# Kernel tuning notes

Measured on AMD Instinct MI355X. Metric: run time of the kernel, lower is better.

The kernel has to match this reference:

```python
import jax, jax.numpy as jnp
import numpy as np

B, C, T = 64, 1, 262144
NUM_BANDS = 6
# (min, max) for each of the 18 normalized control params: 6 bands x (gain_dB, cutoff_Hz, Q)
PARAM_RANGES = np.array([
    [-24.0, 24.0], [20.0, 200.0], [0.1, 10.0],      # low shelf
    [-24.0, 24.0], [200.0, 2000.0], [0.1, 10.0],    # band 1
    [-24.0, 24.0], [200.0, 2000.0], [0.1, 10.0],    # band 2
    [-24.0, 24.0], [2000.0, 8000.0], [0.1, 10.0],   # band 3
    [-24.0, 24.0], [4000.0, 12000.0], [0.1, 10.0],  # band 4
    [-24.0, 24.0], [4000.0, 12000.0], [0.1, 10.0],  # high shelf
], dtype=np.float32)
FILTER_TYPES = ["low_shelf", "peaking", "peaking", "peaking", "peaking", "high_shelf"]


def biquad_coeffs(gain_dB, cutoff, q, sr, ftype):
    # Audio-EQ-cookbook biquad coefficients; all inputs shape (B,)
    A = 10.0 ** (gain_dB / 40.0)
    w0 = 2.0 * jnp.pi * (cutoff / sr)
    alpha = jnp.sin(w0) / (2.0 * q)
    c = jnp.cos(w0)
    sA = jnp.sqrt(A)
    if ftype == "low_shelf":
        b0 = A * ((A + 1) - (A - 1) * c + 2 * sA * alpha)
        b1 = 2 * A * ((A - 1) - (A + 1) * c)
        b2 = A * ((A + 1) - (A - 1) * c - 2 * sA * alpha)
        a0 = (A + 1) + (A - 1) * c + 2 * sA * alpha
        a1 = -2 * ((A - 1) + (A + 1) * c)
        a2 = (A + 1) + (A - 1) * c - 2 * sA * alpha
    elif ftype == "high_shelf":
        b0 = A * ((A + 1) + (A - 1) * c + 2 * sA * alpha)
        b1 = -2 * A * ((A - 1) + (A + 1) * c)
        b2 = A * ((A + 1) + (A - 1) * c - 2 * sA * alpha)
        a0 = (A + 1) - (A - 1) * c + 2 * sA * alpha
        a1 = 2 * ((A - 1) - (A + 1) * c)
        a2 = (A + 1) - (A - 1) * c - 2 * sA * alpha
    else:  # peaking
        b0 = 1 + alpha * A
        b1 = -2 * c
        b2 = 1 - alpha * A
        a0 = 1 + alpha / A
        a1 = -2 * c
        a2 = 1 - alpha / A
    bcoef = jnp.stack([b0, b1, b2], axis=-1) / a0[..., None]  # (B, 3)
    acoef = jnp.stack([a0, a1, a2], axis=-1) / a0[..., None]  # (B, 3)
    return bcoef, acoef


def cascade_biquads(x, bcoefs, acoefs):
    # x: (N, T); bcoefs/acoefs: (6, N, 3). Fused cascade of 6 biquads,
    # direct form II transposed, single scan over time.
    def step(state, xt):  # state: (6, N, 2); xt: (N,)
        v = xt
        new_states = []
        for k in range(NUM_BANDS):
            bk, ak = bcoefs[k], acoefs[k]
            s1, s2 = state[k, :, 0], state[k, :, 1]
            y = bk[:, 0] * v + s1
            ns1 = bk[:, 1] * v - ak[:, 1] * y + s2
            ns2 = bk[:, 2] * v - ak[:, 2] * y
            new_states.append(jnp.stack([ns1, ns2], axis=-1))
            v = y
        return jnp.stack(new_states, axis=0), v
    init = jnp.zeros((NUM_BANDS, x.shape[0], 2), dtype=x.dtype)
    _, y = jax.lax.scan(step, init, x.T)  # y: (T, N)
    return y.T


def setup_inputs() -> dict:
    key = jax.random.key(0)
    k1, k2, k3 = jax.random.split(key, 3)
    x = jax.random.normal(k1, (B, C, T), dtype=jnp.float32) * 0.1
    p = jax.random.normal(k2, (B, 22), dtype=jnp.float32)
    W = jax.random.normal(k3, (18, 22), dtype=jnp.float32) * (1.0 / np.sqrt(22.0))
    b = jnp.zeros((18,), dtype=jnp.float32)
    return {"x": x, "p": p, "W": W, "b": b, "sample_rate": 24000}


def reference(x, p, W, b, sample_rate):
    bs, chs, s = x.shape
    sr = jnp.float32(sample_rate)
    # control path: linear + sigmoid -> 18 normalized params in [0, 1]
    pn = jax.nn.sigmoid(p @ W.T + b)  # (bs, 18)
    lo = jnp.asarray(PARAM_RANGES[:, 0])
    hi = jnp.asarray(PARAM_RANGES[:, 1])
    params = pn * (hi - lo) + lo  # denormalized, (bs, 18)
    bcoefs, acoefs = [], []
    for k, ftype in enumerate(FILTER_TYPES):
        g, f, q = params[:, 3 * k], params[:, 3 * k + 1], params[:, 3 * k + 2]
        bk, ak = biquad_coeffs(g, f, q, sr, ftype)
        bcoefs.append(bk)
        acoefs.append(ak)
    bcoefs = jnp.stack(bcoefs, axis=0)  # (6, bs, 3)
    acoefs = jnp.stack(acoefs, axis=0)
    # share each item's EQ across its channels
    bcoefs = jnp.repeat(bcoefs, chs, axis=1)  # (6, bs*chs, 3)
    acoefs = jnp.repeat(acoefs, chs, axis=1)
    y = cascade_biquads(x.reshape(bs * chs, s), bcoefs, acoefs)
    return y.reshape(bs, chs, s)
```

## Files before the change

kernel.cpp:

```cpp
#include <hip/hip_runtime.h>
#include <math.h>

#define NB    64
#define NT    262144
#define CH    64
#define NCK   (NT/CH)
#define NBANDS 6

#define COEF_OFF 0
#define MAT_OFF  4096
#define T_OFF    (MAT_OFF + NB*1728)
#define WPRE_OFF (T_OFF + NB*64*12)
#define D_OFF    (WPRE_OFF + NB*64*12)

struct Coef { float b0, b1, b2, a1, a2; };

__device__ __forceinline__ float rfl(float x) {
  return __int_as_float(__builtin_amdgcn_readfirstlane(__float_as_int(x)));
}

__device__ __forceinline__ float cascade_step(float v, float s[12], const Coef cf[NBANDS]) {
#pragma unroll
  for (int k = 0; k < NBANDS; ++k) {
    float s1 = s[2*k], s2 = s[2*k+1];
    float y   = fmaf(cf[k].b0, v, s1);
    float ns1 = fmaf(cf[k].b1, v, fmaf(-cf[k].a1, y, s2));
    float ns2 = fmaf(cf[k].b2, v, -cf[k].a2 * y);
    s[2*k]   = ns1;
    s[2*k+1] = ns2;
    v = y;
  }
  return v;
}

__device__ __forceinline__ void load_coefs(const float* ws, int batch, Coef cf[NBANDS]) {
  const float* c = ws + COEF_OFF + batch*30;
#pragma unroll
  for (int k = 0; k < NBANDS; ++k) {
    cf[k].b0 = rfl(c[5*k+0]); cf[k].b1 = rfl(c[5*k+1]); cf[k].b2 = rfl(c[5*k+2]);
    cf[k].a1 = rfl(c[5*k+3]); cf[k].a2 = rfl(c[5*k+4]);
  }
}

__global__ __launch_bounds__(64) void k_prep(const float* __restrict__ p, const float* __restrict__ W,
                                             const float* __restrict__ bias, const int* __restrict__ srp,
                                             float* __restrict__ ws) {
  __shared__ float prmS[18];
  __shared__ float cfS[30];
  __shared__ float M0[144], M1[144];
  int b = blockIdx.x, tid = threadIdx.x;
  const float lo[18] = {-24.f,20.f,0.1f,  -24.f,200.f,0.1f,  -24.f,200.f,0.1f,
                        -24.f,2000.f,0.1f, -24.f,4000.f,0.1f, -24.f,4000.f,0.1f};
  const float hi[18] = { 24.f,200.f,10.f,  24.f,2000.f,10.f,  24.f,2000.f,10.f,
                         24.f,8000.f,10.f, 24.f,12000.f,10.f, 24.f,12000.f,10.f};
  if (tid < 18) {
    float acc = bias[tid];
    for (int j = 0; j < 22; ++j) acc = fmaf(W[tid*22+j], p[b*22+j], acc);
    float sg = 1.f / (1.f + expf(-acc));
    prmS[tid] = sg * (hi[tid] - lo[tid]) + lo[tid];
  }
  __syncthreads();
  if (tid < 6) {
    int k = tid;
    float g = prmS[3*k], f = prmS[3*k+1], q = prmS[3*k+2];
    float sr = (float)srp[0];
    float A  = powf(10.f, g * (1.f/40.f));
    float w0 = 6.28318530717958647692f * (f / sr);
    float al = sinf(w0) / (2.f*q);
    float c  = cosf(w0);
    float sA = sqrtf(A);
    float b0,b1,b2,a0,a1,a2;
    if (k == 0) {
      b0 = A*((A+1.f) - (A-1.f)*c + 2.f*sA*al);
      b1 = 2.f*A*((A-1.f) - (A+1.f)*c);
      b2 = A*((A+1.f) - (A-1.f)*c - 2.f*sA*al);
      a0 = (A+1.f) + (A-1.f)*c + 2.f*sA*al;
      a1 = -2.f*((A-1.f) + (A+1.f)*c);
      a2 = (A+1.f) + (A-1.f)*c - 2.f*sA*al;
    } else if (k == 5) {
      b0 = A*((A+1.f) + (A-1.f)*c + 2.f*sA*al);
      b1 = -2.f*A*((A-1.f) + (A+1.f)*c);
      b2 = A*((A+1.f) + (A-1.f)*c - 2.f*sA*al);
      a0 = (A+1.f) - (A-1.f)*c + 2.f*sA*al;
      a1 = 2.f*((A-1.f) - (A+1.f)*c);
      a2 = (A+1.f) - (A-1.f)*c - 2.f*sA*al;
    } else {
      b0 = 1.f + al*A;
      b1 = -2.f*c;
      b2 = 1.f - al*A;
      a0 = 1.f + al/A;
      a1 = -2.f*c;
      a2 = 1.f - al/A;
    }
    float inv = 1.f/a0;
    float* cws = ws + COEF_OFF + b*30;
    cws[5*k+0] = cfS[5*k+0] = b0*inv;
    cws[5*k+1] = cfS[5*k+1] = b1*inv;
    cws[5*k+2] = cfS[5*k+2] = b2*inv;
    cws[5*k+3] = cfS[5*k+3] = a1*inv;
    cws[5*k+4] = cfS[5*k+4] = a2*inv;
  }
  __syncthreads();

  Coef cf[NBANDS];
#pragma unroll
  for (int k = 0; k < NBANDS; ++k) {
    cf[k].b0 = cfS[5*k+0]; cf[k].b1 = cfS[5*k+1]; cf[k].b2 = cfS[5*k+2];
    cf[k].a1 = cfS[5*k+3]; cf[k].a2 = cfS[5*k+4];
  }
  if (tid < 12) {
    float s[12];
#pragma unroll
    for (int r = 0; r < 12; ++r) s[r] = (r == tid) ? 1.f : 0.f;
    cascade_step(0.f, s, cf);
#pragma unroll
    for (int r = 0; r < 12; ++r) M0[r*12 + tid] = s[r];
  }
  __syncthreads();

  float* S = M0; float* D = M1;
  float* mout = ws + MAT_OFF + (size_t)b*1728;
  for (int q = 0; q < 6; ++q) {
    for (int e = tid; e < 144; e += 64) {
      int r = e/12, c = e%12;
      float acc = 0.f;
#pragma unroll
      for (int k = 0; k < 12; ++k) acc = fmaf(S[r*12+k], S[k*12+c], acc);
      D[e] = acc;
    }
    __syncthreads();
    float* t = S; S = D; D = t;
  }
  for (int e = tid; e < 144; e += 64) mout[e] = S[e];
  for (int l = 1; l < 12; ++l) {
    for (int e = tid; e < 144; e += 64) {
      int r = e/12, c = e%12;
      float acc = 0.f;
#pragma unroll
      for (int k = 0; k < 12; ++k) acc = fmaf(S[r*12+k], S[k*12+c], acc);
      D[e] = acc;
    }
    __syncthreads();
    float* t = S; S = D; D = t;
    for (int e = tid; e < 144; e += 64) mout[l*144 + e] = S[e];
  }
}

__global__ __launch_bounds__(256) void k_passA(const float* __restrict__ x, float* __restrict__ ws) {
  __shared__ float4 buf[4][2][256];
  __shared__ float KM[6][144];
  int tid = threadIdx.x, wib = tid >> 6, lane = tid & 63;
  int gw = blockIdx.x*4 + wib;
  int batch = gw >> 6, wv = gw & 63;
  int batch_b = blockIdx.x >> 4;

  const float* mb = ws + MAT_OFF + (size_t)batch_b*1728;
  for (int e = tid; e < 864; e += 256) KM[e/144][e%144] = mb[e];
  __syncthreads();

  const float4* x4 = (const float4*)x;
  size_t gbase4 = (size_t)batch*65536 + (size_t)wv*1024;
  int r2 = lane >> 2, c2 = lane & 3;
  float4* bufA = buf[wib][0];
  float4* bufB = buf[wib][1];

  float4 va[4], vb[4];
#pragma unroll
  for (int j = 0; j < 4; ++j) va[j] = x4[gbase4 + (size_t)(j*16 + r2)*16 + c2];

  Coef cf[NBANDS];
  load_coefs(ws, batch, cf);
  float s[12];
#pragma unroll
  for (int i = 0; i < 12; ++i) s[i] = 0.f;

#pragma unroll
  for (int j = 0; j < 4; ++j) bufA[c2*64 + j*16 + r2] = va[j];
  asm volatile("s_waitcnt lgkmcnt(0)" ::: "memory");

#pragma unroll
  for (int q = 0; q < 4; ++q) {
    float4* bp = (q & 1) ? bufB : bufA;
    float4* bn = (q & 1) ? bufA : bufB;
    float4* vr = (q & 1) ? va : vb;
    if (q < 3) {
#pragma unroll
      for (int j = 0; j < 4; ++j)
        vr[j] = x4[gbase4 + (size_t)(j*16 + r2)*16 + (q+1)*4 + c2];
    }
#pragma unroll
    for (int t = 0; t < 4; ++t) {
      float4 xv = bp[t*64 + lane];
      cascade_step(xv.x, s, cf);
      cascade_step(xv.y, s, cf);
      cascade_step(xv.z, s, cf);
      cascade_step(xv.w, s, cf);
    }
    if (q < 3) {
#pragma unroll
      for (int j = 0; j < 4; ++j) bn[c2*64 + j*16 + r2] = vr[j];
      asm volatile("s_waitcnt lgkmcnt(0)" ::: "memory");
    }
  }

#pragma unroll
  for (int l = 0; l < 6; ++l) {
    const int pd = 1 << l;
    float nb[12];
#pragma unroll
    for (int r = 0; r < 12; ++r) nb[r] = __shfl_up(s[r], pd);
    if (lane >= pd) {
#pragma unroll
      for (int r = 0; r < 12; ++r) {
        float acc = s[r];
#pragma unroll
        for (int c = 0; c < 12; ++c) acc = fmaf(KM[l][r*12+c], nb[c], acc);
        s[r] = acc;
      }
    }
  }

  if (lane == 63) {
    float4* tp = (float4*)(ws + T_OFF + ((size_t)batch*64 + wv)*12);
    tp[0] = make_float4(s[0], s[1], s[2],  s[3]);
    tp[1] = make_float4(s[4], s[5], s[6],  s[7]);
    tp[2] = make_float4(s[8], s[9], s[10], s[11]);
  }

  float e[12];
#pragma unroll
  for (int r = 0; r < 12; ++r) e[r] = __shfl_up(s[r], 1);
  if (lane == 0) {
#pragma unroll
    for (int r = 0; r < 12; ++r) e[r] = 0.f;
  }
  int chunk = wv*64 + lane;
  float4* dp = (float4*)(ws + D_OFF + ((size_t)batch*NCK + chunk)*12);
  dp[0] = make_float4(e[0], e[1], e[2],  e[3]);
  dp[1] = make_float4(e[4], e[5], e[6],  e[7]);
  dp[2] = make_float4(e[8], e[9], e[10], e[11]);
}

__global__ __launch_bounds__(64) void k_scanW(float* __restrict__ ws) {
  __shared__ float WM[6][144];
  int b = blockIdx.x, lane = threadIdx.x;
  const float* mb = ws + MAT_OFF + (size_t)b*1728 + 864;
  for (int e = lane; e < 864; e += 64) WM[e/144][e%144] = mb[e];
  __syncthreads();

  const float4* tp = (const float4*)(ws + T_OFF + ((size_t)b*64 + lane)*12);
  float4 a0 = tp[0], a1 = tp[1], a2 = tp[2];
  float s[12] = {a0.x,a0.y,a0.z,a0.w, a1.x,a1.y,a1.z,a1.w, a2.x,a2.y,a2.z,a2.w};

#pragma unroll
  for (int l = 0; l < 6; ++l) {
    const int pd = 1 << l;
    float nb[12];
#pragma unroll
    for (int r = 0; r < 12; ++r) nb[r] = __shfl_up(s[r], pd);
    if (lane >= pd) {
#pragma unroll
      for (int r = 0; r < 12; ++r) {
        float acc = s[r];
#pragma unroll
        for (int c = 0; c < 12; ++c) acc = fmaf(WM[l][r*12+c], nb[c], acc);
        s[r] = acc;
      }
    }
  }
  float e[12];
#pragma unroll
  for (int r = 0; r < 12; ++r) e[r] = __shfl_up(s[r], 1);
  if (lane == 0) {
#pragma unroll
    for (int r = 0; r < 12; ++r) e[r] = 0.f;
  }
  float4* wp = (float4*)(ws + WPRE_OFF + ((size_t)b*64 + lane)*12);
  wp[0] = make_float4(e[0], e[1], e[2],  e[3]);
  wp[1] = make_float4(e[4], e[5], e[6],  e[7]);
  wp[2] = make_float4(e[8], e[9], e[10], e[11]);
}

__global__ __launch_bounds__(256) void k_passB(const float* __restrict__ x, const float* __restrict__ ws,
                                               float* __restrict__ out) {
  __shared__ float4 buf[4][2][256];
  __shared__ float KM[6][144];
  int tid = threadIdx.x, wib = tid >> 6, lane = tid & 63;
  int gw = blockIdx.x*4 + wib;
  int batch = gw >> 6, wv = gw & 63;
  int batch_b = blockIdx.x >> 4;

  const float* mb = ws + MAT_OFF + (size_t)batch_b*1728;
  for (int e = tid; e < 864; e += 256) KM[e/144][e%144] = mb[e];
  __syncthreads();

  const float4* x4 = (const float4*)x;
  float4* out4 = (float4*)out;
  size_t gbase4 = (size_t)batch*65536 + (size_t)wv*1024;
  int r2 = lane >> 2, c2 = lane & 3;
  float4* bufA = buf[wib][0];
  float4* bufB = buf[wib][1];

  float4 va[4], vb[4];
#pragma unroll
  for (int j = 0; j < 4; ++j) va[j] = x4[gbase4 + (size_t)(j*16 + r2)*16 + c2];

  Coef cf[NBANDS];
  load_coefs(ws, batch, cf);

  int chunk = wv*64 + lane;
  const float4* dp = (const float4*)(ws + D_OFF + ((size_t)batch*NCK + chunk)*12);
  float4 e0 = dp[0], e1 = dp[1], e2 = dp[2];
  const float4* wp = (const float4*)(ws + WPRE_OFF + ((size_t)batch*64 + wv)*12);
  float4 w0 = wp[0], w1 = wp[1], w2 = wp[2];
  float R[12] = {w0.x,w0.y,w0.z,w0.w, w1.x,w1.y,w1.z,w1.w, w2.x,w2.y,w2.z,w2.w};
#pragma unroll
  for (int l = 0; l < 6; ++l) {
    float t[12];
#pragma unroll
    for (int r = 0; r < 12; ++r) {
      float acc = 0.f;
#pragma unroll
      for (int c = 0; c < 12; ++c) acc = fmaf(KM[l][r*12+c], R[c], acc);
      t[r] = acc;
    }
    bool sel = (lane >> l) & 1;
#pragma unroll
    for (int r = 0; r < 12; ++r) R[r] = sel ? t[r] : R[r];
  }
  float s[12] = {e0.x+R[0], e0.y+R[1], e0.z+R[2],  e0.w+R[3],
                 e1.x+R[4], e1.y+R[5], e1.z+R[6],  e1.w+R[7],
                 e2.x+R[8], e2.y+R[9], e2.z+R[10], e2.w+R[11]};

#pragma unroll
  for (int j = 0; j < 4; ++j) bufA[c2*64 + j*16 + r2] = va[j];
  asm volatile("s_waitcnt lgkmcnt(0)" ::: "memory");

#pragma unroll
  for (int q = 0; q < 4; ++q) {
    float4* bp = (q & 1) ? bufB : bufA;
    float4* bn = (q & 1) ? bufA : bufB;
    float4* vr = (q & 1) ? va : vb;
    if (q < 3) {
#pragma unroll
      for (int j = 0; j < 4; ++j)
        vr[j] = x4[gbase4 + (size_t)(j*16 + r2)*16 + (q+1)*4 + c2];
    }
#pragma unroll
    for (int t = 0; t < 4; ++t) {
      float4 xv = bp[t*64 + lane];
      float4 yv;
      yv.x = cascade_step(xv.x, s, cf);
      yv.y = cascade_step(xv.y, s, cf);
      yv.z = cascade_step(xv.z, s, cf);
      yv.w = cascade_step(xv.w, s, cf);
      bp[t*64 + lane] = yv;
    }
    asm volatile("s_waitcnt lgkmcnt(0)" ::: "memory");
#pragma unroll
    for (int j = 0; j < 4; ++j) {
      float4 w = bp[c2*64 + j*16 + r2];
      out4[gbase4 + (size_t)(j*16 + r2)*16 + q*4 + c2] = w;
    }
    if (q < 3) {
#pragma unroll
      for (int j = 0; j < 4; ++j) bn[c2*64 + j*16 + r2] = vr[j];
      asm volatile("s_waitcnt lgkmcnt(0)" ::: "memory");
    }
  }
}

extern "C" void kernel_launch(void* const* d_in, const int* in_sizes, int n_in,
                              void* d_out, int out_size, void* d_ws, size_t ws_size,
                              hipStream_t stream) {
  const float* x    = (const float*)d_in[0];
  const float* p    = (const float*)d_in[1];
  const float* W    = (const float*)d_in[2];
  const float* bias = (const float*)d_in[3];
  const int*   sr   = (const int*)d_in[4];
  float* ws  = (float*)d_ws;
  float* out = (float*)d_out;

  int passBlocks = (NB * NCK) / 256;
  hipLaunchKernelGGL(k_prep,  dim3(NB),         dim3(64),  0, stream, p, W, bias, sr, ws);
  hipLaunchKernelGGL(k_passA, dim3(passBlocks), dim3(256), 0, stream, x, ws);
  hipLaunchKernelGGL(k_scanW, dim3(NB),         dim3(64),  0, stream, ws);
  hipLaunchKernelGGL(k_passB, dim3(passBlocks), dim3(256), 0, stream, x, ws, out);
}
```

Baseline: 93.59 us.

## Replace sequential per-chunk recurrence in pass A with precomputed impulse-response matvec

In the prep kernel, each batch's 64 state-response vectors (M^(63-t) times the input-injection vector) are now precomputed and written to the workspace. Pass A then computes each chunk's zero-initial-state end state as a linear combination of these vectors with the 64 inputs, using independent FMAs instead of a serial 6-band cascade per sample. This removes the long dependent recurrence and the LDS transpose buffering, at the cost of more FMAs per sample (12 per input) and reads of the shared per-batch vector table. It also changes the load pattern to 16 contiguous float4 per lane, which is less coalesced across lanes.

```diff
diff --git a/kernel.cpp b/kernel.cpp
--- a/kernel.cpp
+++ b/kernel.cpp
@@ -118,9 +118,27 @@
   }
   __syncthreads();
 
+  float w[12];
+#pragma unroll
+  for (int r = 0; r < 12; ++r) w[r] = 0.f;
+  cascade_step(1.f, w, cf);
+  int e63 = 63 - tid;
+
   float* S = M0; float* D = M1;
   float* mout = ws + MAT_OFF + (size_t)b*1728;
   for (int q = 0; q < 6; ++q) {
+    if ((e63 >> q) & 1) {
+      float t[12];
+#pragma unroll
+      for (int r = 0; r < 12; ++r) {
+        float acc = 0.f;
+#pragma unroll
+        for (int k = 0; k < 12; ++k) acc = fmaf(S[r*12+k], w[k], acc);
+        t[r] = acc;
+      }
+#pragma unroll
+      for (int r = 0; r < 12; ++r) w[r] = t[r];
+    }
     for (int e = tid; e < 144; e += 64) {
       int r = e/12, c = e%12;
       float acc = 0.f;
@@ -130,6 +148,11 @@
     }
     __syncthreads();
     float* t = S; S = D; D = t;
+  }
+  {
+    float* vout = ws + WPRE_OFF + (size_t)b*768;
+#pragma unroll
+    for (int r = 0; r < 12; ++r) vout[tid*12 + r] = w[r];
   }
   for (int e = tid; e < 144; e += 64) mout[e] = S[e];
   for (int l = 1; l < 12; ++l) {
@@ -146,8 +169,9 @@
   }
 }
 
-__global__ __launch_bounds__(256) void k_passA(const float* __restrict__ x, float* __restrict__ ws) {
-  __shared__ float4 buf[4][2][256];
+__global__ __launch_bounds__(256) void k_passA(const float* __restrict__ x,
+                                               const float* __restrict__ Vt,
+                                               float* __restrict__ ws) {
   __shared__ float KM[6][144];
   int tid = threadIdx.x, wib = tid >> 6, lane = tid & 63;
   int gw = blockIdx.x*4 + wib;
@@ -158,48 +182,28 @@
   for (int e = tid; e < 864; e += 256) KM[e/144][e%144] = mb[e];
   __syncthreads();
 
-  const float4* x4 = (const float4*)x;
-  size_t gbase4 = (size_t)batch*65536 + (size_t)wv*1024;
-  int r2 = lane >> 2, c2 = lane & 3;
-  float4* bufA = buf[wib][0];
-  float4* bufB = buf[wib][1];
-
-  float4 va[4], vb[4];
-#pragma unroll
-  for (int j = 0; j < 4; ++j) va[j] = x4[gbase4 + (size_t)(j*16 + r2)*16 + c2];
-
-  Coef cf[NBANDS];
-  load_coefs(ws, batch, cf);
+  const float4* xp = (const float4*)x + (size_t)batch*65536 + (size_t)wv*1024 + (size_t)lane*16;
+  const float* Vb = Vt + (size_t)batch_b*768;
+
+  float4 xv[16];
+#pragma unroll
+  for (int k = 0; k < 16; ++k) xv[k] = xp[k];
+
   float s[12];
 #pragma unroll
-  for (int i = 0; i < 12; ++i) s[i] = 0.f;
-
-#pragma unroll
-  for (int j = 0; j < 4; ++j) bufA[c2*64 + j*16 + r2] = va[j];
-  asm volatile("s_waitcnt lgkmcnt(0)" ::: "memory");
-
-#pragma unroll
-  for (int q = 0; q < 4; ++q) {
-    float4* bp = (q & 1) ? bufB : bufA;
-    float4* bn = (q & 1) ? bufA : bufB;
-    float4* vr = (q & 1) ? va : vb;
-    if (q < 3) {
-#pragma unroll
-      for (int j = 0; j < 4; ++j)
-        vr[j] = x4[gbase4 + (size_t)(j*16 + r2)*16 + (q+1)*4 + c2];
-    }
-#pragma unroll
-    for (int t = 0; t < 4; ++t) {
-      float4 xv = bp[t*64 + lane];
-      cascade_step(xv.x, s, cf);
-      cascade_step(xv.y, s, cf);
-      cascade_step(xv.z, s, cf);
-      cascade_step(xv.w, s, cf);
-    }
-    if (q < 3) {
-#pragma unroll
-      for (int j = 0; j < 4; ++j) bn[c2*64 + j*16 + r2] = vr[j];
-      asm volatile("s_waitcnt lgkmcnt(0)" ::: "memory");
+  for (int r = 0; r < 12; ++r) s[r] = 0.f;
+
+#pragma unroll
+  for (int k = 0; k < 16; ++k) {
+    const float* vr = Vb + k*48;
+#pragma unroll
+    for (int r = 0; r < 12; ++r) {
+      float acc = s[r];
+      acc = fmaf(vr[r],      xv[k].x, acc);
+      acc = fmaf(vr[12 + r], xv[k].y, acc);
+      acc = fmaf(vr[24 + r], xv[k].z, acc);
+      acc = fmaf(vr[36 + r], xv[k].w, acc);
+      s[r] = acc;
     }
   }
 
@@ -383,7 +387,7 @@
 
   int passBlocks = (NB * NCK) / 256;
   hipLaunchKernelGGL(k_prep,  dim3(NB),         dim3(64),  0, stream, p, W, bias, sr, ws);
-  hipLaunchKernelGGL(k_passA, dim3(passBlocks), dim3(256), 0, stream, x, ws);
+  hipLaunchKernelGGL(k_passA, dim3(passBlocks), dim3(256), 0, stream, x, ws + WPRE_OFF, ws);
   hipLaunchKernelGGL(k_scanW, dim3(NB),         dim3(64),  0, stream, ws);
   hipLaunchKernelGGL(k_passB, dim3(passBlocks), dim3(256), 0, stream, x, ws, out);
 }
```

New measurement: 97.58 us. 1.04x slower.

## Replace pass-A cascade recurrence with precomputed impulse-response state vectors

Applied to the files above, without the earlier changes.

Pass A computes only the zero-initial-state end state of each 64-sample chunk. Because that state is linear in the inputs, it can be written as a sum of per-sample state vectors (A^(63-t) times the input response). The setup kernel now builds these 64 twelve-element vectors by binary powering alongside the existing matrix squaring and stores them in the workspace. Pass A then accumulates them with 48 independent FMAs per sample instead of running the serial six-biquad cascade. This removes the serial dependency chain, but it adds global/scalar loads of the vectors and changes the floating-point summation order.

```diff
diff --git a/kernel.cpp b/kernel.cpp
--- a/kernel.cpp
+++ b/kernel.cpp
@@ -118,9 +118,27 @@
   }
   __syncthreads();
 
+  float w[12];
+#pragma unroll
+  for (int r = 0; r < 12; ++r) w[r] = 0.f;
+  cascade_step(1.f, w, cf);
+  int e63 = 63 - tid;
+
   float* S = M0; float* D = M1;
   float* mout = ws + MAT_OFF + (size_t)b*1728;
   for (int q = 0; q < 6; ++q) {
+    if ((e63 >> q) & 1) {
+      float t[12];
+#pragma unroll
+      for (int r = 0; r < 12; ++r) {
+        float acc = 0.f;
+#pragma unroll
+        for (int k = 0; k < 12; ++k) acc = fmaf(S[r*12+k], w[k], acc);
+        t[r] = acc;
+      }
+#pragma unroll
+      for (int r = 0; r < 12; ++r) w[r] = t[r];
+    }
     for (int e = tid; e < 144; e += 64) {
       int r = e/12, c = e%12;
       float acc = 0.f;
@@ -130,6 +148,11 @@
     }
     __syncthreads();
     float* t = S; S = D; D = t;
+  }
+  {
+    float* vout = ws + WPRE_OFF + (size_t)b*768;
+#pragma unroll
+    for (int r = 0; r < 12; ++r) vout[tid*12 + r] = w[r];
   }
   for (int e = tid; e < 144; e += 64) mout[e] = S[e];
   for (int l = 1; l < 12; ++l) {
@@ -163,13 +186,12 @@
   int r2 = lane >> 2, c2 = lane & 3;
   float4* bufA = buf[wib][0];
   float4* bufB = buf[wib][1];
+  const float* Vb = ws + WPRE_OFF + (size_t)batch_b*768;
 
   float4 va[4], vb[4];
 #pragma unroll
   for (int j = 0; j < 4; ++j) va[j] = x4[gbase4 + (size_t)(j*16 + r2)*16 + c2];
 
-  Coef cf[NBANDS];
-  load_coefs(ws, batch, cf);
   float s[12];
 #pragma unroll
   for (int i = 0; i < 12; ++i) s[i] = 0.f;
@@ -191,10 +213,16 @@
 #pragma unroll
     for (int t = 0; t < 4; ++t) {
       float4 xv = bp[t*64 + lane];
-      cascade_step(xv.x, s, cf);
-      cascade_step(xv.y, s, cf);
-      cascade_step(xv.z, s, cf);
-      cascade_step(xv.w, s, cf);
+      const float* vrow = Vb + (q*4 + t)*48;
+#pragma unroll
+      for (int r = 0; r < 12; ++r) {
+        float acc = s[r];
+        acc = fmaf(vrow[r],      xv.x, acc);
+        acc = fmaf(vrow[12 + r], xv.y, acc);
+        acc = fmaf(vrow[24 + r], xv.z, acc);
+        acc = fmaf(vrow[36 + r], xv.w, acc);
+        s[r] = acc;
+      }
     }
     if (q < 3) {
 #pragma unroll
```

Measured after the change: 106.2 us. 1.13x slower.
